# Kernel optimization log

Measured on AMD Instinct MI355X. Metric: run time of the kernel, lower is better.

## Reference

```python
import jax, jax.numpy as jnp
import numpy as np

NUM_EXPERTS = 64
TOP_K = 2
CAPACITY_FACTOR = 1.25
D_MODEL = 2048
BATCH, SEQ = 4, 4096


def setup_inputs() -> dict:
    key = jax.random.key(0)
    kx, kw = jax.random.split(key)
    x = jax.random.normal(kx, (BATCH, SEQ, D_MODEL), dtype=jnp.float32)
    # router weight: Linear(input_dim, num_experts, bias=False), init std=0.001
    W = jax.random.normal(kw, (NUM_EXPERTS, D_MODEL), dtype=jnp.float32) * 0.001
    return {"x": x, "W": W}


def reference(x, W):
    B, S, D = x.shape
    N = B * S  # combined batch of tokens
    E = NUM_EXPERTS
    k = TOP_K
    capacity = int(CAPACITY_FACTOR * N * k / E)  # static Python int

    x_flat = x.reshape(N, D)
    router_logits = jnp.einsum('nd,ed->ne', x_flat, W)  # [N, E]
    routing_weights = jax.nn.softmax(router_logits, axis=-1)

    top_k_weights, top_k_indices = jax.lax.top_k(routing_weights, k)  # [N, k]
    top_k_weights = top_k_weights / (top_k_weights.sum(-1, keepdims=True) + 1e-8)

    expert_counts = jnp.zeros((E,), dtype=jnp.float32)
    dispatch_mask = jnp.zeros((N, E), dtype=jnp.float32)
    token_ids = jnp.arange(N)

    # Sequential over k (fixed, small): within a k-step the capacity check uses
    # counts from previous steps only, matching the torch scatter semantics.
    for k_idx in range(k):
        expert_idx = top_k_indices[:, k_idx]            # [N]
        under_cap = expert_counts[expert_idx] < capacity  # [N] bool
        expert_counts = expert_counts + jax.ops.segment_sum(
            under_cap.astype(jnp.float32), expert_idx, num_segments=E)
        # top-k experts are distinct per token, so add == set on zero-init slots
        dispatch_mask = dispatch_mask.at[token_ids, expert_idx].add(
            jnp.where(under_cap, top_k_weights[:, k_idx], 0.0))

    # Tokens that got dropped everywhere go to the least-loaded expert with w=1
    unrouted = dispatch_mask.sum(-1) == 0                     # [N]
    least_loaded = jnp.argmax(capacity - expert_counts)       # scalar
    dispatch_mask = jnp.where(
        unrouted[:, None] & (jnp.arange(E)[None, :] == least_loaded),
        1.0, dispatch_mask)

    normalized_dispatch_mask = dispatch_mask / (dispatch_mask.sum(-1, keepdims=True) + 1e-8)

    router_z_loss = jnp.mean(jnp.square(router_logits))
    counts = normalized_dispatch_mask.sum(0)                  # [E]
    target_count = float(N * k / E)
    load_balance_loss = jnp.mean(jnp.square(counts / float(N) - target_count / float(N)))
    router_loss = 0.001 * jax.lax.stop_gradient(router_z_loss) \
                + 0.001 * jax.lax.stop_gradient(load_balance_loss)

    return (jax.lax.stop_gradient(routing_weights), normalized_dispatch_mask, router_loss)
```

## Files before the change

### kernel.cpp

```cpp
#include <hip/hip_runtime.h>
#include <math.h>

#define N_TOK 16384
#define D_MODEL 2048
#define N_EXP 64
#define CAPACITY 640
#define NREP 8

#define BK 32
#define NSTAGE (D_MODEL / BK)
#define LP 48

typedef __attribute__((ext_vector_type(8))) _Float16 h8;
typedef __attribute__((ext_vector_type(4))) float f4;

__global__ __launch_bounds__(256, 1) void k12_gemm_softmax(
    const float* __restrict__ x, const float* __restrict__ W,
    float* __restrict__ rw_out, int2* __restrict__ top12,
    float2* __restrict__ wts, int* __restrict__ histR,
    float* __restrict__ zR) {
  __shared__ _Float16 XH[2][64][LP];
  __shared__ _Float16 XL[2][64][LP];
  __shared__ _Float16 WHs[2][64][LP];
  __shared__ _Float16 WLs[2][64][LP];
  __shared__ float slog[64][65];
  __shared__ float zred[4];

  const int t = threadIdx.x;
  const int lane = t & 63;
  const int wid = t >> 6;
  const int m0 = blockIdx.x * 64;
  const int rep = blockIdx.x & (NREP - 1);

  const int srow = t >> 2;
  const int scol = (t & 3) * 8;
  const float* xg = x + (size_t)(m0 + srow) * D_MODEL + scol;
  const float* wg = W + (size_t)srow * D_MODEL + scol;

  float4 xa0 = *(const float4*)(xg);
  float4 xa1 = *(const float4*)(xg + 4);
  float4 wa0 = *(const float4*)(wg);
  float4 wa1 = *(const float4*)(wg + 4);
  float4 xb0 = *(const float4*)(xg + BK);
  float4 xb1 = *(const float4*)(xg + BK + 4);
  float4 wb0 = *(const float4*)(wg + BK);
  float4 wb1 = *(const float4*)(wg + BK + 4);

  f4 acc1[4], acc2[4];
#pragma unroll
  for (int i = 0; i < 4; i++) {
    acc1[i] = (f4)(0.f);
    acc2[i] = (f4)(0.f);
  }

#define CVT_STORE(buf, X0, X1, W0, W1)                              \
  {                                                                 \
    float xv[8] = {X0.x, X0.y, X0.z, X0.w, X1.x, X1.y, X1.z, X1.w}; \
    float wv[8] = {W0.x, W0.y, W0.z, W0.w, W1.x, W1.y, W1.z, W1.w}; \
    h8 cxh, cxl, cwh, cwl;                                          \
    _Pragma("unroll") for (int j = 0; j < 8; j++) {                 \
      _Float16 h = (_Float16)xv[j];                                 \
      cxh[j] = h;                                                   \
      cxl[j] = (_Float16)((xv[j] - (float)h) * 1024.f);             \
      float wsc = wv[j] * 1024.f;                                   \
      _Float16 hw = (_Float16)wsc;                                  \
      cwh[j] = hw;                                                  \
      cwl[j] = (_Float16)((wsc - (float)hw) * 1024.f);              \
    }                                                               \
    *(h8*)&XH[buf][srow][scol] = cxh;                               \
    *(h8*)&XL[buf][srow][scol] = cxl;                               \
    *(h8*)&WHs[buf][srow][scol] = cwh;                              \
    *(h8*)&WLs[buf][srow][scol] = cwl;                              \
  }

#define COMPUTE(buf)                                                          \
  {                                                                           \
    const int frow = lane & 15;                                               \
    const int fk = (lane >> 4) * 8;                                           \
    h8 ah = *(const h8*)&XH[buf][wid * 16 + frow][fk];                        \
    h8 al = *(const h8*)&XL[buf][wid * 16 + frow][fk];                        \
    _Pragma("unroll") for (int nt = 0; nt < 4; nt++) {                        \
      h8 bh = *(const h8*)&WHs[buf][nt * 16 + frow][fk];                      \
      h8 bl = *(const h8*)&WLs[buf][nt * 16 + frow][fk];                      \
      acc1[nt] =                                                              \
          __builtin_amdgcn_mfma_f32_16x16x32_f16(ah, bh, acc1[nt], 0, 0, 0);  \
      acc2[nt] =                                                              \
          __builtin_amdgcn_mfma_f32_16x16x32_f16(al, bh, acc2[nt], 0, 0, 0);  \
      acc2[nt] =                                                              \
          __builtin_amdgcn_mfma_f32_16x16x32_f16(ah, bl, acc2[nt], 0, 0, 0);  \
    }                                                                         \
  }

  CVT_STORE(0, xa0, xa1, wa0, wa1);
  for (int it = 0; it < NSTAGE / 2; it++) {
    __syncthreads();
    const int s2 = 2 * it + 2;
    if (s2 < NSTAGE) {
      xa0 = *(const float4*)(xg + s2 * BK);
      xa1 = *(const float4*)(xg + s2 * BK + 4);
      wa0 = *(const float4*)(wg + s2 * BK);
      wa1 = *(const float4*)(wg + s2 * BK + 4);
    }
    COMPUTE(0);
    CVT_STORE(1, xb0, xb1, wb0, wb1);
    __syncthreads();
    const int s3 = 2 * it + 3;
    if (s3 < NSTAGE) {
      xb0 = *(const float4*)(xg + s3 * BK);
      xb1 = *(const float4*)(xg + s3 * BK + 4);
      wb0 = *(const float4*)(wg + s3 * BK);
      wb1 = *(const float4*)(wg + s3 * BK + 4);
    }
    COMPUTE(1);
    if (it + 1 < NSTAGE / 2) CVT_STORE(0, xa0, xa1, wa0, wa1);
  }

  const int cg = lane >> 4, ci = lane & 15;
#pragma unroll
  for (int nt = 0; nt < 4; nt++)
#pragma unroll
    for (int r = 0; r < 4; r++) {
      const float v =
          (acc1[nt][r] + acc2[nt][r] * 0.0009765625f) * 0.0009765625f;
      slog[wid * 16 + cg * 4 + r][nt * 16 + ci] = v;
    }

  float z_acc = 0.f;
  for (int tt = 0; tt < 16; tt++) {
    const int tloc = wid * 16 + tt;
    const int n = m0 + tloc;
    const float v = slog[tloc][lane];
    z_acc += v * v;
    float mx = v;
#pragma unroll
    for (int off = 32; off; off >>= 1) mx = fmaxf(mx, __shfl_xor(mx, off));
    const float p = __expf(v - mx);
    float ssum = p;
#pragma unroll
    for (int off = 32; off; off >>= 1) ssum += __shfl_xor(ssum, off);
    const float rw = p / ssum;
    rw_out[(size_t)n * N_EXP + lane] = rw;

    const unsigned long long b1 = __ballot(v == mx);
    const int i1 = __builtin_ctzll(b1);
    float v2 = (lane == i1) ? -INFINITY : v;
#pragma unroll
    for (int off = 32; off; off >>= 1) v2 = fmaxf(v2, __shfl_xor(v2, off));
    const unsigned long long b2 = __ballot(v == v2) & ~(1ull << i1);
    const int i2 = __builtin_ctzll(b2);
    const float rw1 = __shfl(rw, i1);
    const float rw2 = __shfl(rw, i2);
    if (lane == 0) {
      const float denom = rw1 + rw2 + 1e-8f;
      top12[n] = make_int2(i1, i2);
      wts[n] = make_float2(rw1 / denom, rw2 / denom);
      atomicAdd(&histR[(rep * N_EXP + i1) * 16], 1);
    }
  }
#pragma unroll
  for (int off = 32; off; off >>= 1) z_acc += __shfl_xor(z_acc, off);
  if (lane == 0) zred[wid] = z_acc;
  __syncthreads();
  if (t == 0) atomicAdd(&zR[rep * 16], zred[0] + zred[1] + zred[2] + zred[3]);
}

__global__ __launch_bounds__(256) void k3_dispatch(
    const int2* __restrict__ top12, const float2* __restrict__ wts,
    const int* __restrict__ histR, float* __restrict__ mask_out,
    float* __restrict__ cntR) {
  const int lane = threadIdx.x & 63;
  const int wid = threadIdx.x >> 6;
  const int n = blockIdx.x * 4 + wid;
  const int rep = blockIdx.x & (NREP - 1);

  const int2 ij = top12[n];
  const float2 w = wts[n];
  int h = 0;
#pragma unroll
  for (int r = 0; r < NREP; r++) h += histR[(r * N_EXP + ij.y) * 16];
  const bool allowed = h < CAPACITY;
  const float ssum = w.x + (allowed ? w.y : 0.f);
  const float inv = 1.f / (ssum + 1e-8f);
  float val = 0.f;
  if (lane == ij.x) val = w.x * inv;
  else if (allowed && lane == ij.y) val = w.y * inv;
  mask_out[(size_t)n * N_EXP + lane] = val;
  if (val != 0.f) atomicAdd(&cntR[(rep * N_EXP + lane) * 16], val);
}

__global__ void k4_loss(const float* __restrict__ cntR,
                        const float* __restrict__ zR,
                        float* __restrict__ loss_out) {
  const int lane = threadIdx.x;
  float c = 0.f;
#pragma unroll
  for (int r = 0; r < NREP; r++) c += cntR[(r * N_EXP + lane) * 16];
  const float d = (c - 512.0f) * (1.0f / 16384.0f);
  float v = d * d;
#pragma unroll
  for (int off = 32; off; off >>= 1) v += __shfl_xor(v, off);
  if (lane == 0) {
    float z = 0.f;
#pragma unroll
    for (int r = 0; r < NREP; r++) z += zR[r * 16];
    const float lb = v * (1.0f / 64.0f);
    loss_out[0] = 0.001f * (z * (1.0f / (16384.0f * 64.0f))) + 0.001f * lb;
  }
}

extern "C" void kernel_launch(void* const* d_in, const int* in_sizes, int n_in,
                              void* d_out, int out_size, void* d_ws,
                              size_t ws_size, hipStream_t stream) {
  const float* x = (const float*)d_in[0];
  const float* W = (const float*)d_in[1];
  float* out = (float*)d_out;
  float* rw_out = out;
  float* mask_out = out + (size_t)N_TOK * N_EXP;
  float* loss_out = out + 2 * (size_t)N_TOK * N_EXP;

  char* ws = (char*)d_ws;
  int* histR = (int*)ws;
  float* cntR = (float*)(ws + 32768);
  float* zR = (float*)(ws + 65536);
  int2* top12 = (int2*)(ws + 131072);
  float2* wts = (float2*)(ws + 262144);

  hipMemsetAsync(histR, 0, 65536 + 512, stream);
  k12_gemm_softmax<<<256, 256, 0, stream>>>(x, W, rw_out, top12, wts, histR,
                                            zR);
  k3_dispatch<<<N_TOK / 4, 256, 0, stream>>>(top12, wts, histR, mask_out,
                                             cntR);
  k4_loss<<<1, 64, 0, stream>>>(cntR, zR, loss_out);
}
```

Baseline: 223.7 us.

## Load X MFMA fragments directly into registers, widen K-tile, single sync per stage

Result: slower. 228.5 us (+2.2%).

```diff
diff --git a/kernel.cpp b/kernel.cpp
--- a/kernel.cpp
+++ b/kernel.cpp
@@ -7,9 +7,9 @@
 #define CAPACITY 640
 #define NREP 8
 
-#define BK 32
+#define BK 64
 #define NSTAGE (D_MODEL / BK)
-#define LP 48
+#define LPW 72
 
 typedef __attribute__((ext_vector_type(8))) _Float16 h8;
 typedef __attribute__((ext_vector_type(4))) float f4;
@@ -19,10 +19,8 @@
     float* __restrict__ rw_out, int2* __restrict__ top12,
     float2* __restrict__ wts, int* __restrict__ histR,
     float* __restrict__ zR) {
-  __shared__ _Float16 XH[2][64][LP];
-  __shared__ _Float16 XL[2][64][LP];
-  __shared__ _Float16 WHs[2][64][LP];
-  __shared__ _Float16 WLs[2][64][LP];
+  __shared__ __align__(16) _Float16 WHs[2][64][LPW];
+  __shared__ __align__(16) _Float16 WLs[2][64][LPW];
   __shared__ float slog[64][65];
   __shared__ float zred[4];
 
@@ -32,20 +30,16 @@
   const int m0 = blockIdx.x * 64;
   const int rep = blockIdx.x & (NREP - 1);
 
-  const int srow = t >> 2;
-  const int scol = (t & 3) * 8;
-  const float* xg = x + (size_t)(m0 + srow) * D_MODEL + scol;
-  const float* wg = W + (size_t)srow * D_MODEL + scol;
-
-  float4 xa0 = *(const float4*)(xg);
-  float4 xa1 = *(const float4*)(xg + 4);
-  float4 wa0 = *(const float4*)(wg);
-  float4 wa1 = *(const float4*)(wg + 4);
-  float4 xb0 = *(const float4*)(xg + BK);
-  float4 xb1 = *(const float4*)(xg + BK + 4);
-  float4 wb0 = *(const float4*)(wg + BK);
-  float4 wb1 = *(const float4*)(wg + BK + 4);
-
+  const int we = t >> 2;
+  const int wc = (t & 3) * 16;
+  const int frow = lane & 15;
+  const int fk = (lane >> 4) * 8;
+
+  const float* wg = W + (size_t)we * D_MODEL + wc;
+  const float* xg = x + (size_t)(m0 + wid * 16 + frow) * D_MODEL + fk;
+
+  float4 wreg[2][4], xreg[2][4];
+  h8 afh[2][2], afl[2][2];
   f4 acc1[4], acc2[4];
 #pragma unroll
   for (int i = 0; i < 4; i++) {
@@ -53,66 +47,109 @@
     acc2[i] = (f4)(0.f);
   }
 
-#define CVT_STORE(buf, X0, X1, W0, W1)                              \
-  {                                                                 \
-    float xv[8] = {X0.x, X0.y, X0.z, X0.w, X1.x, X1.y, X1.z, X1.w}; \
-    float wv[8] = {W0.x, W0.y, W0.z, W0.w, W1.x, W1.y, W1.z, W1.w}; \
-    h8 cxh, cxl, cwh, cwl;                                          \
-    _Pragma("unroll") for (int j = 0; j < 8; j++) {                 \
-      _Float16 h = (_Float16)xv[j];                                 \
-      cxh[j] = h;                                                   \
-      cxl[j] = (_Float16)((xv[j] - (float)h) * 1024.f);             \
-      float wsc = wv[j] * 1024.f;                                   \
-      _Float16 hw = (_Float16)wsc;                                  \
-      cwh[j] = hw;                                                  \
-      cwl[j] = (_Float16)((wsc - (float)hw) * 1024.f);              \
-    }                                                               \
-    *(h8*)&XH[buf][srow][scol] = cxh;                               \
-    *(h8*)&XL[buf][srow][scol] = cxl;                               \
-    *(h8*)&WHs[buf][srow][scol] = cwh;                              \
-    *(h8*)&WLs[buf][srow][scol] = cwl;                              \
-  }
-
-#define COMPUTE(buf)                                                          \
-  {                                                                           \
-    const int frow = lane & 15;                                               \
-    const int fk = (lane >> 4) * 8;                                           \
-    h8 ah = *(const h8*)&XH[buf][wid * 16 + frow][fk];                        \
-    h8 al = *(const h8*)&XL[buf][wid * 16 + frow][fk];                        \
-    _Pragma("unroll") for (int nt = 0; nt < 4; nt++) {                        \
-      h8 bh = *(const h8*)&WHs[buf][nt * 16 + frow][fk];                      \
-      h8 bl = *(const h8*)&WLs[buf][nt * 16 + frow][fk];                      \
-      acc1[nt] =                                                              \
-          __builtin_amdgcn_mfma_f32_16x16x32_f16(ah, bh, acc1[nt], 0, 0, 0);  \
-      acc2[nt] =                                                              \
-          __builtin_amdgcn_mfma_f32_16x16x32_f16(al, bh, acc2[nt], 0, 0, 0);  \
-      acc2[nt] =                                                              \
-          __builtin_amdgcn_mfma_f32_16x16x32_f16(ah, bl, acc2[nt], 0, 0, 0);  \
-    }                                                                         \
-  }
-
-  CVT_STORE(0, xa0, xa1, wa0, wa1);
-  for (int it = 0; it < NSTAGE / 2; it++) {
-    __syncthreads();
-    const int s2 = 2 * it + 2;
-    if (s2 < NSTAGE) {
-      xa0 = *(const float4*)(xg + s2 * BK);
-      xa1 = *(const float4*)(xg + s2 * BK + 4);
-      wa0 = *(const float4*)(wg + s2 * BK);
-      wa1 = *(const float4*)(wg + s2 * BK + 4);
-    }
-    COMPUTE(0);
-    CVT_STORE(1, xb0, xb1, wb0, wb1);
-    __syncthreads();
-    const int s3 = 2 * it + 3;
-    if (s3 < NSTAGE) {
-      xb0 = *(const float4*)(xg + s3 * BK);
-      xb1 = *(const float4*)(xg + s3 * BK + 4);
-      wb0 = *(const float4*)(wg + s3 * BK);
-      wb1 = *(const float4*)(wg + s3 * BK + 4);
-    }
-    COMPUTE(1);
-    if (it + 1 < NSTAGE / 2) CVT_STORE(0, xa0, xa1, wa0, wa1);
+#define LOAD_W(slot, s)                        \
+  {                                            \
+    const float* p_ = wg + (s) * BK;           \
+    wreg[slot][0] = *(const float4*)(p_);      \
+    wreg[slot][1] = *(const float4*)(p_ + 4);  \
+    wreg[slot][2] = *(const float4*)(p_ + 8);  \
+    wreg[slot][3] = *(const float4*)(p_ + 12); \
+  }
+#define LOAD_X(slot, s)                        \
+  {                                            \
+    const float* p_ = xg + (s) * BK;           \
+    xreg[slot][0] = *(const float4*)(p_);      \
+    xreg[slot][1] = *(const float4*)(p_ + 4);  \
+    xreg[slot][2] = *(const float4*)(p_ + 32); \
+    xreg[slot][3] = *(const float4*)(p_ + 36); \
+  }
+
+#define CVTSTORE_W(slot, buf)                                           \
+  {                                                                     \
+    float wf[16] = {wreg[slot][0].x, wreg[slot][0].y, wreg[slot][0].z,  \
+                    wreg[slot][0].w, wreg[slot][1].x, wreg[slot][1].y,  \
+                    wreg[slot][1].z, wreg[slot][1].w, wreg[slot][2].x,  \
+                    wreg[slot][2].y, wreg[slot][2].z, wreg[slot][2].w,  \
+                    wreg[slot][3].x, wreg[slot][3].y, wreg[slot][3].z,  \
+                    wreg[slot][3].w};                                   \
+    h8 h0, h1, l0, l1;                                                  \
+    _Pragma("unroll") for (int j = 0; j < 8; j++) {                     \
+      float s0 = wf[j] * 1024.f;                                        \
+      _Float16 a_ = (_Float16)s0;                                       \
+      h0[j] = a_;                                                       \
+      l0[j] = (_Float16)((s0 - (float)a_) * 1024.f);                    \
+      float s1 = wf[j + 8] * 1024.f;                                    \
+      _Float16 b_ = (_Float16)s1;                                       \
+      h1[j] = b_;                                                       \
+      l1[j] = (_Float16)((s1 - (float)b_) * 1024.f);                    \
+    }                                                                   \
+    *(h8*)&WHs[buf][we][wc] = h0;                                       \
+    *(h8*)&WHs[buf][we][wc + 8] = h1;                                   \
+    *(h8*)&WLs[buf][we][wc] = l0;                                       \
+    *(h8*)&WLs[buf][we][wc + 8] = l1;                                   \
+  }
+
+#define CVT_X(slot)                                                    \
+  {                                                                    \
+    float xf[16] = {xreg[slot][0].x, xreg[slot][0].y, xreg[slot][0].z, \
+                    xreg[slot][0].w, xreg[slot][1].x, xreg[slot][1].y, \
+                    xreg[slot][1].z, xreg[slot][1].w, xreg[slot][2].x, \
+                    xreg[slot][2].y, xreg[slot][2].z, xreg[slot][2].w, \
+                    xreg[slot][3].x, xreg[slot][3].y, xreg[slot][3].z, \
+                    xreg[slot][3].w};                                  \
+    _Pragma("unroll") for (int j = 0; j < 8; j++) {                    \
+      _Float16 a_ = (_Float16)xf[j];                                   \
+      afh[slot][0][j] = a_;                                            \
+      afl[slot][0][j] = (_Float16)((xf[j] - (float)a_) * 1024.f);      \
+      _Float16 b_ = (_Float16)xf[j + 8];                               \
+      afh[slot][1][j] = b_;                                            \
+      afl[slot][1][j] = (_Float16)((xf[j + 8] - (float)b_) * 1024.f);  \
+    }                                                                  \
+  }
+
+#define COMPUTE(buf, p)                                                      \
+  {                                                                          \
+    _Pragma("unroll") for (int ks = 0; ks < 2; ks++) {                       \
+      _Pragma("unroll") for (int nt = 0; nt < 4; nt++) {                     \
+        h8 bh = *(const h8*)&WHs[buf][nt * 16 + frow][ks * 32 + fk];         \
+        h8 bl = *(const h8*)&WLs[buf][nt * 16 + frow][ks * 32 + fk];         \
+        acc1[nt] = __builtin_amdgcn_mfma_f32_16x16x32_f16(afh[p][ks], bh,    \
+                                                          acc1[nt], 0, 0, 0); \
+        acc2[nt] = __builtin_amdgcn_mfma_f32_16x16x32_f16(afl[p][ks], bh,    \
+                                                          acc2[nt], 0, 0, 0); \
+        acc2[nt] = __builtin_amdgcn_mfma_f32_16x16x32_f16(afh[p][ks], bl,    \
+                                                          acc2[nt], 0, 0, 0); \
+      }                                                                      \
+    }                                                                        \
+  }
+
+#define PHASE(p, s)                 \
+  {                                 \
+    if ((s) + 1 < NSTAGE) {         \
+      CVTSTORE_W(1 - (p), 1 - (p)); \
+      CVT_X(1 - (p));               \
+    }                               \
+    if ((s) + 3 < NSTAGE) {         \
+      LOAD_W(1 - (p), (s) + 3);     \
+      LOAD_X(1 - (p), (s) + 3);     \
+    }                               \
+    COMPUTE((p), (p));              \
+    __syncthreads();                \
+  }
+
+  LOAD_W(0, 0);
+  LOAD_X(0, 0);
+  LOAD_W(1, 1);
+  LOAD_X(1, 1);
+  CVTSTORE_W(0, 0);
+  CVT_X(0);
+  LOAD_W(0, 2);
+  LOAD_X(0, 2);
+  __syncthreads();
+
+  for (int it = 0; it < NSTAGE; it += 2) {
+    PHASE(0, it);
+    PHASE(1, it + 1);
   }
 
   const int cg = lane >> 4, ci = lane & 15;
```

## Pre-split W into fp16 fragments and stream tiles via global_load_lds

Applied to the files above, without the earlier changes.

New measurement: 228.9 us. 1.02x slower.

```diff
diff --git a/kernel.cpp b/kernel.cpp
--- a/kernel.cpp
+++ b/kernel.cpp
@@ -6,128 +6,132 @@
 #define N_EXP 64
 #define CAPACITY 640
 #define NREP 8
-
-#define BK 32
-#define NSTAGE (D_MODEL / BK)
-#define LP 48
+#define TM 32
+#define NSTEP 32
 
 typedef __attribute__((ext_vector_type(8))) _Float16 h8;
 typedef __attribute__((ext_vector_type(4))) float f4;
 
-__global__ __launch_bounds__(256, 1) void k12_gemm_softmax(
-    const float* __restrict__ x, const float* __restrict__ W,
+#define AS1 __attribute__((address_space(1)))
+#define AS3 __attribute__((address_space(3)))
+__device__ __forceinline__ void gld16(const void* g, void* l) {
+  __builtin_amdgcn_global_load_lds((const AS1 void*)g, (AS3 void*)l, 16, 0, 0);
+}
+
+__global__ __launch_bounds__(256) void k0_cvtw(const float* __restrict__ W,
+                                               _Float16* __restrict__ WT) {
+  const int lane = threadIdx.x & 63;
+  const int c = blockIdx.x * 4 + (threadIdx.x >> 6);
+  const int s = c >> 4, q = c & 15;
+  const int part = q >> 3, ks = (q >> 2) & 1, nt = q & 3;
+  const int e = nt * 16 + (lane & 15);
+  const int k = s * 64 + ks * 32 + (lane >> 4) * 8;
+  const float* src = W + (size_t)e * D_MODEL + k;
+  const float4 a = *(const float4*)src;
+  const float4 b = *(const float4*)(src + 4);
+  const float f[8] = {a.x, a.y, a.z, a.w, b.x, b.y, b.z, b.w};
+  h8 out;
+#pragma unroll
+  for (int j = 0; j < 8; j++) {
+    const float sc = f[j] * 1024.f;
+    const _Float16 h = (_Float16)sc;
+    out[j] = part ? (_Float16)((sc - (float)h) * 1024.f) : h;
+  }
+  *(h8*)(WT + (size_t)c * 512 + lane * 8) = out;
+}
+
+__global__ __launch_bounds__(256, 2) void k12_gemm_softmax(
+    const float* __restrict__ x, const _Float16* __restrict__ WT,
     float* __restrict__ rw_out, int2* __restrict__ top12,
     float2* __restrict__ wts, int* __restrict__ histR,
     float* __restrict__ zR) {
-  __shared__ _Float16 XH[2][64][LP];
-  __shared__ _Float16 XL[2][64][LP];
-  __shared__ _Float16 WHs[2][64][LP];
-  __shared__ _Float16 WLs[2][64][LP];
-  __shared__ float slog[64][65];
+  __shared__ __align__(16) float XS[2][2048];
+  __shared__ __align__(16) _Float16 WS[2][8192];
+  __shared__ float slog[TM][65];
   __shared__ float zred[4];
 
   const int t = threadIdx.x;
   const int lane = t & 63;
   const int wid = t >> 6;
-  const int m0 = blockIdx.x * 64;
+  const int m0 = blockIdx.x * TM;
   const int rep = blockIdx.x & (NREP - 1);
 
-  const int srow = t >> 2;
-  const int scol = (t & 3) * 8;
-  const float* xg = x + (size_t)(m0 + srow) * D_MODEL + scol;
-  const float* wg = W + (size_t)srow * D_MODEL + scol;
-
-  float4 xa0 = *(const float4*)(xg);
-  float4 xa1 = *(const float4*)(xg + 4);
-  float4 wa0 = *(const float4*)(wg);
-  float4 wa1 = *(const float4*)(wg + 4);
-  float4 xb0 = *(const float4*)(xg + BK);
-  float4 xb1 = *(const float4*)(xg + BK + 4);
-  float4 wb0 = *(const float4*)(wg + BK);
-  float4 wb1 = *(const float4*)(wg + BK + 4);
-
-  f4 acc1[4], acc2[4];
-#pragma unroll
-  for (int i = 0; i < 4; i++) {
+  const int i0 = wid * 2;
+  const int r0 = i0 * 4 + (lane >> 4);
+  const int r1 = r0 + 4;
+  const int s16 = lane & 15;
+  const float* xs0 = x + (size_t)(m0 + r0) * D_MODEL + ((s16 ^ (r0 & 7)) * 4);
+  const float* xs1 = x + (size_t)(m0 + r1) * D_MODEL + ((s16 ^ (r1 & 7)) * 4);
+  const _Float16* wsrc = WT + (size_t)(wid * 4) * 512 + lane * 8;
+
+  f4 acc1[2], acc2[2];
+#pragma unroll
+  for (int i = 0; i < 2; i++) {
     acc1[i] = (f4)(0.f);
     acc2[i] = (f4)(0.f);
   }
 
-#define CVT_STORE(buf, X0, X1, W0, W1)                              \
-  {                                                                 \
-    float xv[8] = {X0.x, X0.y, X0.z, X0.w, X1.x, X1.y, X1.z, X1.w}; \
-    float wv[8] = {W0.x, W0.y, W0.z, W0.w, W1.x, W1.y, W1.z, W1.w}; \
-    h8 cxh, cxl, cwh, cwl;                                          \
-    _Pragma("unroll") for (int j = 0; j < 8; j++) {                 \
-      _Float16 h = (_Float16)xv[j];                                 \
-      cxh[j] = h;                                                   \
-      cxl[j] = (_Float16)((xv[j] - (float)h) * 1024.f);             \
-      float wsc = wv[j] * 1024.f;                                   \
-      _Float16 hw = (_Float16)wsc;                                  \
-      cwh[j] = hw;                                                  \
-      cwl[j] = (_Float16)((wsc - (float)hw) * 1024.f);              \
-    }                                                               \
-    *(h8*)&XH[buf][srow][scol] = cxh;                               \
-    *(h8*)&XL[buf][srow][scol] = cxl;                               \
-    *(h8*)&WHs[buf][srow][scol] = cwh;                              \
-    *(h8*)&WLs[buf][srow][scol] = cwl;                              \
-  }
-
-#define COMPUTE(buf)                                                          \
-  {                                                                           \
-    const int frow = lane & 15;                                               \
-    const int fk = (lane >> 4) * 8;                                           \
-    h8 ah = *(const h8*)&XH[buf][wid * 16 + frow][fk];                        \
-    h8 al = *(const h8*)&XL[buf][wid * 16 + frow][fk];                        \
-    _Pragma("unroll") for (int nt = 0; nt < 4; nt++) {                        \
-      h8 bh = *(const h8*)&WHs[buf][nt * 16 + frow][fk];                      \
-      h8 bl = *(const h8*)&WLs[buf][nt * 16 + frow][fk];                      \
-      acc1[nt] =                                                              \
-          __builtin_amdgcn_mfma_f32_16x16x32_f16(ah, bh, acc1[nt], 0, 0, 0);  \
-      acc2[nt] =                                                              \
-          __builtin_amdgcn_mfma_f32_16x16x32_f16(al, bh, acc2[nt], 0, 0, 0);  \
-      acc2[nt] =                                                              \
-          __builtin_amdgcn_mfma_f32_16x16x32_f16(ah, bl, acc2[nt], 0, 0, 0);  \
-    }                                                                         \
-  }
-
-  CVT_STORE(0, xa0, xa1, wa0, wa1);
-  for (int it = 0; it < NSTAGE / 2; it++) {
+#define STAGE(buf, s)                                           \
+  {                                                             \
+    gld16(xs0 + (s) * 64, &XS[buf][i0 * 256]);                  \
+    gld16(xs1 + (s) * 64, &XS[buf][i0 * 256 + 256]);            \
+    _Pragma("unroll") for (int j2 = 0; j2 < 4; j2++)            \
+        gld16(wsrc + (size_t)(s) * 8192 + j2 * 512,             \
+              &WS[buf][(wid * 4 + j2) * 512]);                  \
+  }
+
+#define COMPUTE(buf)                                                           \
+  {                                                                            \
+    _Pragma("unroll") for (int ks = 0; ks < 2; ks++) {                         \
+      const h8 bh = *(const h8*)&WS[buf][(ks * 4 + wid) * 512 + lane * 8];     \
+      const h8 bl = *(const h8*)&WS[buf][(8 + ks * 4 + wid) * 512 + lane * 8]; \
+      _Pragma("unroll") for (int mf = 0; mf < 2; mf++) {                       \
+        const int row = mf * 16 + (lane & 15);                                 \
+        const int cb = ks * 8 + (lane >> 4) * 2;                               \
+        const int sw = lane & 7;                                               \
+        const f4 a0 = *(const f4*)&XS[buf][row * 64 + ((cb ^ sw) * 4)];        \
+        const f4 a1 = *(const f4*)&XS[buf][row * 64 + (((cb + 1) ^ sw) * 4)];  \
+        h8 ah, al;                                                             \
+        const float xf[8] = {a0[0], a0[1], a0[2], a0[3],                       \
+                             a1[0], a1[1], a1[2], a1[3]};                      \
+        _Pragma("unroll") for (int j = 0; j < 8; j++) {                        \
+          const _Float16 hv = (_Float16)xf[j];                                 \
+          ah[j] = hv;                                                          \
+          al[j] = (_Float16)((xf[j] - (float)hv) * 1024.f);                    \
+        }                                                                      \
+        acc1[mf] = __builtin_amdgcn_mfma_f32_16x16x32_f16(ah, bh, acc1[mf],    \
+                                                          0, 0, 0);            \
+        acc2[mf] = __builtin_amdgcn_mfma_f32_16x16x32_f16(al, bh, acc2[mf],    \
+                                                          0, 0, 0);            \
+        acc2[mf] = __builtin_amdgcn_mfma_f32_16x16x32_f16(ah, bl, acc2[mf],    \
+                                                          0, 0, 0);            \
+      }                                                                        \
+    }                                                                          \
+  }
+
+  STAGE(0, 0);
+  int cur = 0;
+  for (int s = 0; s < NSTEP; s++) {
     __syncthreads();
-    const int s2 = 2 * it + 2;
-    if (s2 < NSTAGE) {
-      xa0 = *(const float4*)(xg + s2 * BK);
-      xa1 = *(const float4*)(xg + s2 * BK + 4);
-      wa0 = *(const float4*)(wg + s2 * BK);
-      wa1 = *(const float4*)(wg + s2 * BK + 4);
-    }
-    COMPUTE(0);
-    CVT_STORE(1, xb0, xb1, wb0, wb1);
-    __syncthreads();
-    const int s3 = 2 * it + 3;
-    if (s3 < NSTAGE) {
-      xb0 = *(const float4*)(xg + s3 * BK);
-      xb1 = *(const float4*)(xg + s3 * BK + 4);
-      wb0 = *(const float4*)(wg + s3 * BK);
-      wb1 = *(const float4*)(wg + s3 * BK + 4);
-    }
-    COMPUTE(1);
-    if (it + 1 < NSTAGE / 2) CVT_STORE(0, xa0, xa1, wa0, wa1);
+    if (s + 1 < NSTEP) STAGE(cur ^ 1, s + 1);
+    COMPUTE(cur);
+    cur ^= 1;
   }
 
   const int cg = lane >> 4, ci = lane & 15;
 #pragma unroll
-  for (int nt = 0; nt < 4; nt++)
+  for (int mf = 0; mf < 2; mf++)
 #pragma unroll
     for (int r = 0; r < 4; r++) {
       const float v =
-          (acc1[nt][r] + acc2[nt][r] * 0.0009765625f) * 0.0009765625f;
-      slog[wid * 16 + cg * 4 + r][nt * 16 + ci] = v;
+          (acc1[mf][r] + acc2[mf][r] * 0.0009765625f) * 0.0009765625f;
+      slog[mf * 16 + cg * 4 + r][wid * 16 + ci] = v;
     }
+  __syncthreads();
 
   float z_acc = 0.f;
-  for (int tt = 0; tt < 16; tt++) {
-    const int tloc = wid * 16 + tt;
+  for (int tt = 0; tt < 8; tt++) {
+    const int tloc = wid * 8 + tt;
     const int n = m0 + tloc;
     const float v = slog[tloc][lane];
     z_acc += v * v;
@@ -224,9 +228,11 @@
   float* zR = (float*)(ws + 65536);
   int2* top12 = (int2*)(ws + 131072);
   float2* wts = (float2*)(ws + 262144);
+  _Float16* WT = (_Float16*)(ws + 393216);
 
   hipMemsetAsync(histR, 0, 65536 + 512, stream);
-  k12_gemm_softmax<<<256, 256, 0, stream>>>(x, W, rw_out, top12, wts, histR,
+  k0_cvtw<<<128, 256, 0, stream>>>(W, WT);
+  k12_gemm_softmax<<<512, 256, 0, stream>>>(x, WT, rw_out, top12, wts, histR,
                                             zR);
   k3_dispatch<<<N_TOK / 4, 256, 0, stream>>>(top12, wts, histR, mask_out,
                                              cntR);
```
